# Performance work log

Hardware: AMD Instinct MI355X
Metric: run time of the kernel (lower is better)

## Reference

```python
import jax, jax.numpy as jnp
import numpy as np

B, S, C = 2, 4096, 512
H = 8            # num heads
D = C // H       # head dim = 64


def setup_inputs() -> dict:
    key = jax.random.key(0)
    ks = jax.random.split(key, 5)
    s = 0.02
    return {
        "hidden_states": jax.random.normal(ks[0], (B, S, C), dtype=jnp.float32),
        "Wq": jax.random.normal(ks[1], (C, C), dtype=jnp.float32) * s,
        "Wk": jax.random.normal(ks[2], (C, C), dtype=jnp.float32) * s,
        "Wv": jax.random.normal(ks[3], (C, C), dtype=jnp.float32) * s,
        "Wo": jax.random.normal(ks[4], (C, C), dtype=jnp.float32) * s,
        "bo": jnp.zeros((C,), dtype=jnp.float32),
    }


def reference(hidden_states, Wq, Wk, Wv, Wo, bo):
    # Self-attention path of AttnProcessor (encoder_hidden_states=None,
    # no norms, no mask, residual_connection=False, rescale=1.0).
    b, s, c = hidden_states.shape
    scale = jnp.float32(D) ** -0.5
    # QKV projections (Linear, no bias as in diffusers defaults)
    q = hidden_states @ Wq.T   # [b,s,c]
    k = hidden_states @ Wk.T
    v = hidden_states @ Wv.T
    # head_to_batch_dim: [b,s,c] -> [b,s,h,d]
    q = q.reshape(b, s, H, D)
    k = k.reshape(b, s, H, D)
    v = v.reshape(b, s, H, D)
    # get_attention_scores: scaled QK^T + softmax (full O(S^2) matrix, as in source)
    scores = jnp.einsum("bqhd,bkhd->bhqk", q, k) * scale   # [b,h,s,s]
    probs = jax.nn.softmax(scores, axis=-1)
    # bmm with V, batch_to_head_dim
    out = jnp.einsum("bhqk,bkhd->bqhd", probs, v).reshape(b, s, c)
    # to_out[0] (Linear with bias); to_out[1] is Dropout (identity at eval)
    out = out @ Wo.T + bo
    return out
```

## Files before the change

### kernel.cpp

```cpp
#include <hip/hip_runtime.h>
#include <hip/hip_bf16.h>

#define BB 2
#define SS 4096
#define CC 512
#define HH 8
#define DD 64
#define MM (BB*SS)

typedef __bf16 bf16;
typedef __attribute__((ext_vector_type(8))) __bf16 bf16x8;
typedef __attribute__((ext_vector_type(4))) __bf16 bf16x4;
typedef __attribute__((ext_vector_type(4))) float f32x4;

#define LP 72
#define QSCALE 0.18033688f

__device__ __forceinline__ bf16x8 cvt8(const float4 a, const float4 b) {
  bf16x8 r;
  r[0]=(bf16)a.x; r[1]=(bf16)a.y; r[2]=(bf16)a.z; r[3]=(bf16)a.w;
  r[4]=(bf16)b.x; r[5]=(bf16)b.y; r[6]=(bf16)b.z; r[7]=(bf16)b.w;
  return r;
}

__device__ __forceinline__ void gl16(const bf16* g, bf16* l) {
  __builtin_amdgcn_global_load_lds(
      (const __attribute__((address_space(1))) void*)g,
      (__attribute__((address_space(3))) void*)l, 16, 0, 0);
}

__global__ __launch_bounds__(256) void cvt_all(
    const float* __restrict__ hs, const float* __restrict__ Wq,
    const float* __restrict__ Wk, const float* __restrict__ Wv,
    const float* __restrict__ Wo,
    bf16* __restrict__ Xb, bf16* __restrict__ Wb, bf16* __restrict__ Wob)
{
  const size_t tid = (size_t)blockIdx.x * 256 + threadIdx.x;
  if (tid < 524288) {
    const size_t e = tid * 8;
    float4 a = ((const float4*)(hs + e))[0];
    float4 b = ((const float4*)(hs + e))[1];
    *(bf16x8*)(Xb + e) = cvt8(a, b);
  } else {
    const size_t e = (tid - 524288) * 8;
    if (e < 786432) {
      const int tens = (int)(e >> 18);
      const float* src = ((tens == 0) ? Wq : (tens == 1) ? Wk : Wv) + (e & 262143);
      const float sc = (tens == 0) ? QSCALE : 1.f;
      float4 a = ((const float4*)src)[0];
      float4 b = ((const float4*)src)[1];
      bf16x8 r;
      r[0]=(bf16)(a.x*sc); r[1]=(bf16)(a.y*sc); r[2]=(bf16)(a.z*sc); r[3]=(bf16)(a.w*sc);
      r[4]=(bf16)(b.x*sc); r[5]=(bf16)(b.y*sc); r[6]=(bf16)(b.z*sc); r[7]=(bf16)(b.w*sc);
      *(bf16x8*)(Wb + e) = r;
    } else {
      const size_t eo = e - 786432;
      float4 a = ((const float4*)(Wo + eo))[0];
      float4 b = ((const float4*)(Wo + eo))[1];
      *(bf16x8*)(Wob + eo) = cvt8(a, b);
    }
  }
}

__global__ __launch_bounds__(256) void qkv_gemm(
    const bf16* __restrict__ Xb, const bf16* __restrict__ Wb,
    bf16* __restrict__ qp, bf16* __restrict__ kp, bf16* __restrict__ vtp)
{
  __shared__ bf16 Aa[64*64];
  __shared__ bf16 Ab[64*64];
  __shared__ bf16 Ba[64*64];
  __shared__ bf16 Bb[64*64];
  const int bid = blockIdx.x;
  const int swz = (bid & 7) * 96 + (bid >> 3);
  const int m0  = (swz / 12) * 128;
  const int nf0 = (swz % 12) * 128;
  const int tens = nf0 >> 9;
  const int n0 = nf0 & 511;

  const int t = threadIdx.x;
  const int w = t >> 6;
  const int lane = t & 63;
  const int l15 = lane & 15;
  const int quad = lane >> 4;
  const int sr = lane >> 3;
  const int sc = (lane & 7) * 8;

  f32x4 acc[2][2][4];
  #pragma unroll
  for (int mi = 0; mi < 2; ++mi)
    #pragma unroll
    for (int ni = 0; ni < 2; ++ni)
      #pragma unroll
      for (int nt = 0; nt < 4; ++nt)
        #pragma unroll
        for (int r = 0; r < 4; ++r) acc[mi][ni][nt][r] = 0.f;

  for (int k0 = 0; k0 < CC; k0 += 64) {
    __syncthreads();
    {
      const bf16* pa = Xb + (size_t)(m0 + w*16 + sr) * CC + k0 + sc;
      gl16(pa,             &Aa[w*1024]);
      gl16(pa + 8*CC,      &Aa[w*1024 + 512]);
      const bf16* pb = Xb + (size_t)(m0 + 64 + w*16 + sr) * CC + k0 + sc;
      gl16(pb,             &Ab[w*1024]);
      gl16(pb + 8*CC,      &Ab[w*1024 + 512]);
      const bf16* p1 = Wb + (size_t)(nf0 + w*16 + sr) * CC + k0 + sc;
      gl16(p1,             &Ba[w*1024]);
      gl16(p1 + 8*CC,      &Ba[w*1024 + 512]);
      const bf16* p2 = Wb + (size_t)(nf0 + 64 + w*16 + sr) * CC + k0 + sc;
      gl16(p2,             &Bb[w*1024]);
      gl16(p2 + 8*CC,      &Bb[w*1024 + 512]);
    }
    __syncthreads();
    #pragma unroll
    for (int c = 0; c < 2; ++c) {
      bf16x8 afa = *(const bf16x8*)&Aa[(w*16 + l15)*64 + c*32 + quad*8];
      bf16x8 afb = *(const bf16x8*)&Ab[(w*16 + l15)*64 + c*32 + quad*8];
      #pragma unroll
      for (int nt = 0; nt < 4; ++nt) {
        bf16x8 ba = *(const bf16x8*)&Ba[(nt*16 + l15)*64 + c*32 + quad*8];
        bf16x8 bb = *(const bf16x8*)&Bb[(nt*16 + l15)*64 + c*32 + quad*8];
        acc[0][0][nt] = __builtin_amdgcn_mfma_f32_16x16x32_bf16(afa, ba, acc[0][0][nt], 0, 0, 0);
        acc[1][0][nt] = __builtin_amdgcn_mfma_f32_16x16x32_bf16(afb, ba, acc[1][0][nt], 0, 0, 0);
        acc[0][1][nt] = __builtin_amdgcn_mfma_f32_16x16x32_bf16(afa, bb, acc[0][1][nt], 0, 0, 0);
        acc[1][1][nt] = __builtin_amdgcn_mfma_f32_16x16x32_bf16(afb, bb, acc[1][1][nt], 0, 0, 0);
      }
    }
  }

  bf16* plane = (tens == 0) ? qp : ((tens == 1) ? kp : vtp);
  const int c8 = (t & 7) * 8;

  auto epi = [&](const f32x4* as, int mt0, int nb) {
    const int b = mt0 >> 12, s0g = mt0 & 4095;
    const int h = nb >> 6;
    __syncthreads();
    if (tens < 2) {
      #pragma unroll
      for (int nt = 0; nt < 4; ++nt)
        #pragma unroll
        for (int r = 0; r < 4; ++r)
          Aa[(w*16 + quad*4 + r)*64 + nt*16 + l15] = (bf16)as[nt][r];
    } else {
      #pragma unroll
      for (int nt = 0; nt < 4; ++nt)
        #pragma unroll
        for (int r = 0; r < 4; ++r)
          Aa[(nt*16 + l15)*64 + w*16 + quad*4 + r] = (bf16)as[nt][r];
    }
    __syncthreads();
    #pragma unroll
    for (int i = 0; i < 2; ++i) {
      const int row = (t >> 3) + 32*i;
      bf16x8 v = *(const bf16x8*)&Aa[row*64 + c8];
      if (tens < 2) {
        *(bf16x8*)&plane[((size_t)((b*HH + h)*SS) + s0g + row)*DD + c8] = v;
      } else {
        *(bf16x8*)&plane[((size_t)((b*HH + h)*DD) + row)*SS + s0g + c8] = v;
      }
    }
  };

  epi(acc[0][0], m0,      n0);
  epi(acc[1][0], m0 + 64, n0);
  epi(acc[0][1], m0,      n0 + 64);
  epi(acc[1][1], m0 + 64, n0 + 64);
}

__global__ __launch_bounds__(512, 4) void attn_fa(
    const bf16* __restrict__ qpl, const bf16* __restrict__ kpl,
    const bf16* __restrict__ vtpl, bf16* __restrict__ aout)
{
  __shared__ __align__(16) bf16 smem[2 * 4 * 64 * LP];

  const int t = threadIdx.x;
  const int w = t >> 6;
  const int g = w >> 2;
  const int wl = w & 3;
  const int lane = t & 63;
  const int l15 = lane & 15;
  const int quad = lane >> 4;

  const int lin = blockIdx.x;
  const int bh = lin & 15;
  const int q0 = (lin >> 4) * 128;
  const size_t plane = (size_t)SS * DD;
  const bf16* Qp = qpl + (size_t)bh * plane;
  const bf16* Kp = kpl + (size_t)bh * plane;
  const bf16* Vg = vtpl + (size_t)bh * plane;

  bf16* Ktg = smem + g * (4*64*LP);
  bf16* Vtg = Ktg + 2*64*LP;

  bf16x8 qf[2][2];
  #pragma unroll
  for (int wq = 0; wq < 2; ++wq) {
    const bf16* qr = Qp + (size_t)(q0 + wl*32 + wq*16 + l15) * DD + quad*8;
    qf[wq][0] = *(const bf16x8*)qr;
    qf[wq][1] = *(const bf16x8*)(qr + 32);
  }

  f32x4 o[2][4];
  f32x4 osum[2];
  #pragma unroll
  for (int wq = 0; wq < 2; ++wq) {
    #pragma unroll
    for (int nt = 0; nt < 4; ++nt)
      #pragma unroll
      for (int r = 0; r < 4; ++r) o[wq][nt][r] = 0.f;
    #pragma unroll
    for (int r = 0; r < 4; ++r) osum[wq][r] = 0.f;
  }

  bf16x8 ones;
  #pragma unroll
  for (int i = 0; i < 8; ++i) ones[i] = (bf16)1.0f;

  const int t8  = t & 255;
  const int r0s = t8 >> 2;
  const int cs  = (t8 & 3) << 4;
  const int K0  = ((t8 & 1) << 3) + (((t8 >> 1) & 1) << 5);
  const int kbase = g << 11;

  bf16x8 ka0, ka1, va, vb;
  {
    ka0 = *(const bf16x8*)&Kp[(size_t)(kbase + r0s)*DD + cs];
    ka1 = *(const bf16x8*)&Kp[(size_t)(kbase + r0s)*DD + cs + 8];
    va  = *(const bf16x8*)&Vg[(size_t)r0s*SS + kbase + K0];
    vb  = *(const bf16x8*)&Vg[(size_t)r0s*SS + kbase + K0 + 16];
    *(bf16x8*)&Ktg[r0s*LP + cs]     = ka0;
    *(bf16x8*)&Ktg[r0s*LP + cs + 8] = ka1;
    bf16x8 vv;
    vv[0]=va[0]; vv[1]=va[1]; vv[2]=va[2]; vv[3]=va[3];
    vv[4]=vb[0]; vv[5]=vb[1]; vv[6]=vb[2]; vv[7]=vb[3];
    *(bf16x8*)&Vtg[r0s*LP + cs] = vv;
    vv[0]=va[4]; vv[1]=va[5]; vv[2]=va[6]; vv[3]=va[7];
    vv[4]=vb[4]; vv[5]=vb[5]; vv[6]=vb[6]; vv[7]=vb[7];
    *(bf16x8*)&Vtg[r0s*LP + cs + 8] = vv;
  }
  __syncthreads();

  for (int it = 0; it < 32; ++it) {
    const int cur = it & 1;
    if (it < 31) {
      const int kn = kbase + (it + 1) * 64;
      ka0 = *(const bf16x8*)&Kp[(size_t)(kn + r0s)*DD + cs];
      ka1 = *(const bf16x8*)&Kp[(size_t)(kn + r0s)*DD + cs + 8];
      va  = *(const bf16x8*)&Vg[(size_t)r0s*SS + kn + K0];
      vb  = *(const bf16x8*)&Vg[(size_t)r0s*SS + kn + K0 + 16];
    }

    const bf16* Ktc = Ktg + cur*(64*LP);
    const bf16* Vtc = Vtg + cur*(64*LP);

    f32x4 st[2][4];
    __builtin_amdgcn_s_setprio(1);
    #pragma unroll
    for (int nt = 0; nt < 4; ++nt) {
      bf16x8 kf0 = *(const bf16x8*)&Ktc[(nt*16 + l15)*LP + quad*8];
      bf16x8 kf1 = *(const bf16x8*)&Ktc[(nt*16 + l15)*LP + 32 + quad*8];
      #pragma unroll
      for (int wq = 0; wq < 2; ++wq) {
        f32x4 z; z[0]=z[1]=z[2]=z[3]=0.f;
        z = __builtin_amdgcn_mfma_f32_16x16x32_bf16(kf0, qf[wq][0], z, 0, 0, 0);
        z = __builtin_amdgcn_mfma_f32_16x16x32_bf16(kf1, qf[wq][1], z, 0, 0, 0);
        st[wq][nt] = z;
      }
    }
    __builtin_amdgcn_s_setprio(0);

    bf16x8 pb0[2];
    #pragma unroll
    for (int wq = 0; wq < 2; ++wq)
      #pragma unroll
      for (int nt = 0; nt < 2; ++nt)
        #pragma unroll
        for (int r = 0; r < 4; ++r)
          pb0[wq][(nt & 1)*4 + r] = (bf16)__builtin_amdgcn_exp2f(st[wq][nt][r]);

    __builtin_amdgcn_s_setprio(1);
    #pragma unroll
    for (int nt = 0; nt < 4; ++nt) {
      bf16x8 vf = *(const bf16x8*)&Vtc[(nt*16 + l15)*LP + quad*8];
      #pragma unroll
      for (int wq = 0; wq < 2; ++wq)
        o[wq][nt] = __builtin_amdgcn_mfma_f32_16x16x32_bf16(vf, pb0[wq], o[wq][nt], 0, 0, 0);
    }
    #pragma unroll
    for (int wq = 0; wq < 2; ++wq)
      osum[wq] = __builtin_amdgcn_mfma_f32_16x16x32_bf16(ones, pb0[wq], osum[wq], 0, 0, 0);
    __builtin_amdgcn_s_setprio(0);

    bf16x8 pb1[2];
    #pragma unroll
    for (int wq = 0; wq < 2; ++wq)
      #pragma unroll
      for (int nt = 2; nt < 4; ++nt)
        #pragma unroll
        for (int r = 0; r < 4; ++r)
          pb1[wq][(nt & 1)*4 + r] = (bf16)__builtin_amdgcn_exp2f(st[wq][nt][r]);

    __builtin_amdgcn_s_setprio(1);
    #pragma unroll
    for (int nt = 0; nt < 4; ++nt) {
      bf16x8 vf = *(const bf16x8*)&Vtc[(nt*16 + l15)*LP + 32 + quad*8];
      #pragma unroll
      for (int wq = 0; wq < 2; ++wq)
        o[wq][nt] = __builtin_amdgcn_mfma_f32_16x16x32_bf16(vf, pb1[wq], o[wq][nt], 0, 0, 0);
    }
    #pragma unroll
    for (int wq = 0; wq < 2; ++wq)
      osum[wq] = __builtin_amdgcn_mfma_f32_16x16x32_bf16(ones, pb1[wq], osum[wq], 0, 0, 0);
    __builtin_amdgcn_s_setprio(0);

    if (it < 31) {
      const int nxt = cur ^ 1;
      bf16* Ktn = Ktg + nxt*(64*LP);
      bf16* Vtn = Vtg + nxt*(64*LP);
      *(bf16x8*)&Ktn[r0s*LP + cs]     = ka0;
      *(bf16x8*)&Ktn[r0s*LP + cs + 8] = ka1;
      bf16x8 vv;
      vv[0]=va[0]; vv[1]=va[1]; vv[2]=va[2]; vv[3]=va[3];
      vv[4]=vb[0]; vv[5]=vb[1]; vv[6]=vb[2]; vv[7]=vb[3];
      *(bf16x8*)&Vtn[r0s*LP + cs] = vv;
      vv[0]=va[4]; vv[1]=va[5]; vv[2]=va[6]; vv[3]=va[7];
      vv[4]=vb[4]; vv[5]=vb[5]; vv[6]=vb[6]; vv[7]=vb[7];
      *(bf16x8*)&Vtn[r0s*LP + cs + 8] = vv;
      __syncthreads();
    }
  }

  __syncthreads();
  float* stash = (float*)smem;
  const int sidx = (wl*64 + lane) * 36;
  if (g == 1) {
    #pragma unroll
    for (int wq = 0; wq < 2; ++wq)
      #pragma unroll
      for (int nt = 0; nt < 4; ++nt)
        *(f32x4*)&stash[sidx + (wq*4 + nt)*4] = o[wq][nt];
    stash[sidx + 32] = osum[0][0];
    stash[sidx + 33] = osum[1][0];
  }
  __syncthreads();
  if (g == 0) {
    #pragma unroll
    for (int wq = 0; wq < 2; ++wq)
      #pragma unroll
      for (int nt = 0; nt < 4; ++nt) {
        f32x4 p = *(const f32x4*)&stash[sidx + (wq*4 + nt)*4];
        #pragma unroll
        for (int r = 0; r < 4; ++r) o[wq][nt][r] += p[r];
      }
    const float s0 = osum[0][0] + stash[sidx + 32];
    const float s1 = osum[1][0] + stash[sidx + 33];

    const int b = bh >> 3, h = bh & 7;
    #pragma unroll
    for (int wq = 0; wq < 2; ++wq) {
      const float inv = 1.f / (wq == 0 ? s0 : s1);
      const size_t row = (size_t)(b*SS + q0 + wl*32 + wq*16 + l15) * CC + h*DD;
      #pragma unroll
      for (int nt = 0; nt < 4; ++nt) {
        bf16x4 ov;
        #pragma unroll
        for (int r = 0; r < 4; ++r) ov[r] = (bf16)(o[wq][nt][r] * inv);
        *(bf16x4*)&aout[row + nt*16 + quad*4] = ov;
      }
    }
  }
}

__global__ __launch_bounds__(256) void out_gemm(
    const bf16* __restrict__ A, const bf16* __restrict__ Wob,
    const float* __restrict__ bo, float* __restrict__ out)
{
  __shared__ bf16 Aa[64*64];
  __shared__ bf16 Ab[64*64];
  __shared__ bf16 Bt[64*64];
  const int bid = blockIdx.x;
  const int swz = (bid & 7) * 64 + (bid >> 3);
  const int m0 = (swz >> 3) * 128;
  const int n0 = (swz & 7) * 64;

  const int t = threadIdx.x;
  const int w = t >> 6;
  const int lane = t & 63;
  const int l15 = lane & 15;
  const int quad = lane >> 4;
  const int sr = lane >> 3;
  const int sc = (lane & 7) * 8;

  f32x4 aca[4], acb[4];
  #pragma unroll
  for (int i = 0; i < 4; ++i)
    #pragma unroll
    for (int j = 0; j < 4; ++j) { aca[i][j] = 0.f; acb[i][j] = 0.f; }

  for (int k0 = 0; k0 < CC; k0 += 64) {
    __syncthreads();
    {
      const bf16* pa = A + (size_t)(m0 + w*16 + sr) * CC + k0 + sc;
      gl16(pa,        &Aa[w*1024]);
      gl16(pa + 8*CC, &Aa[w*1024 + 512]);
      const bf16* pb = A + (size_t)(m0 + 64 + w*16 + sr) * CC + k0 + sc;
      gl16(pb,        &Ab[w*1024]);
      gl16(pb + 8*CC, &Ab[w*1024 + 512]);
      const bf16* p1 = Wob + (size_t)(n0 + w*16 + sr) * CC + k0 + sc;
      gl16(p1,        &Bt[w*1024]);
      gl16(p1 + 8*CC, &Bt[w*1024 + 512]);
    }
    __syncthreads();
    #pragma unroll
    for (int c = 0; c < 2; ++c) {
      bf16x8 afa = *(const bf16x8*)&Aa[(w*16 + l15)*64 + c*32 + quad*8];
      bf16x8 afb = *(const bf16x8*)&Ab[(w*16 + l15)*64 + c*32 + quad*8];
      #pragma unroll
      for (int nt = 0; nt < 4; ++nt) {
        bf16x8 bfr = *(const bf16x8*)&Bt[(nt*16 + l15)*64 + c*32 + quad*8];
        aca[nt] = __builtin_amdgcn_mfma_f32_16x16x32_bf16(afa, bfr, aca[nt], 0, 0, 0);
        acb[nt] = __builtin_amdgcn_mfma_f32_16x16x32_bf16(afb, bfr, acb[nt], 0, 0, 0);
      }
    }
  }

  #pragma unroll
  for (int nt = 0; nt < 4; ++nt) {
    const int ng = n0 + nt*16 + l15;
    const float bias = bo[ng];
    #pragma unroll
    for (int r = 0; r < 4; ++r) {
      const int mga = m0 + w*16 + quad*4 + r;
      out[(size_t)mga*CC + ng] = aca[nt][r] + bias;
      const int mgb = m0 + 64 + w*16 + quad*4 + r;
      out[(size_t)mgb*CC + ng] = acb[nt][r] + bias;
    }
  }
}

extern "C" void kernel_launch(void* const* d_in, const int* in_sizes, int n_in,
                              void* d_out, int out_size, void* d_ws, size_t ws_size,
                              hipStream_t stream) {
  const float* hs = (const float*)d_in[0];
  const float* Wq = (const float*)d_in[1];
  const float* Wk = (const float*)d_in[2];
  const float* Wv = (const float*)d_in[3];
  const float* Wo = (const float*)d_in[4];
  const float* bo = (const float*)d_in[5];
  float* out = (float*)d_out;

  const size_t PE = (size_t)BB*HH*SS*DD;
  bf16* ws   = (bf16*)d_ws;
  bf16* qp   = ws;
  bf16* kp   = ws + PE;
  bf16* vtp  = ws + 2*PE;
  bf16* Xb   = ws + 3*PE;
  bf16* aout = ws + 3*PE;
  bf16* Wb   = ws + 4*PE;
  bf16* Wob  = Wb + 786432;

  cvt_all <<<dim3(2560), 256, 0, stream>>>(hs, Wq, Wk, Wv, Wo, Xb, Wb, Wob);
  qkv_gemm<<<dim3(768),  256, 0, stream>>>(Xb, Wb, qp, kp, vtp);
  attn_fa <<<dim3(512),  512, 0, stream>>>(qp, kp, vtp, aout);
  out_gemm<<<dim3(512),  256, 0, stream>>>(aout, Wob, bo, out);
}
```

Measured before the change: 191.0 us.

## Fuse activation fp32-to-bf16 conversion into QKV GEMM and coalesce output stores

After: 192.9 us. Within noise of the previous version (+1.0%).

```diff
diff --git a/kernel.cpp b/kernel.cpp
--- a/kernel.cpp
+++ b/kernel.cpp
@@ -29,45 +29,36 @@
       (__attribute__((address_space(3))) void*)l, 16, 0, 0);
 }
 
-__global__ __launch_bounds__(256) void cvt_all(
-    const float* __restrict__ hs, const float* __restrict__ Wq,
-    const float* __restrict__ Wk, const float* __restrict__ Wv,
-    const float* __restrict__ Wo,
-    bf16* __restrict__ Xb, bf16* __restrict__ Wb, bf16* __restrict__ Wob)
+__global__ __launch_bounds__(256) void cvt_w(
+    const float* __restrict__ Wq, const float* __restrict__ Wk,
+    const float* __restrict__ Wv, const float* __restrict__ Wo,
+    bf16* __restrict__ Wb, bf16* __restrict__ Wob)
 {
-  const size_t tid = (size_t)blockIdx.x * 256 + threadIdx.x;
-  if (tid < 524288) {
-    const size_t e = tid * 8;
-    float4 a = ((const float4*)(hs + e))[0];
-    float4 b = ((const float4*)(hs + e))[1];
-    *(bf16x8*)(Xb + e) = cvt8(a, b);
+  size_t e = ((size_t)blockIdx.x * 256 + threadIdx.x) * 8;
+  if (e < 786432) {
+    const int tens = (int)(e >> 18);
+    const float* src = ((tens == 0) ? Wq : (tens == 1) ? Wk : Wv) + (e & 262143);
+    const float sc = (tens == 0) ? QSCALE : 1.f;
+    float4 a = ((const float4*)src)[0];
+    float4 b = ((const float4*)src)[1];
+    bf16x8 r;
+    r[0]=(bf16)(a.x*sc); r[1]=(bf16)(a.y*sc); r[2]=(bf16)(a.z*sc); r[3]=(bf16)(a.w*sc);
+    r[4]=(bf16)(b.x*sc); r[5]=(bf16)(b.y*sc); r[6]=(bf16)(b.z*sc); r[7]=(bf16)(b.w*sc);
+    *(bf16x8*)(Wb + e) = r;
   } else {
-    const size_t e = (tid - 524288) * 8;
-    if (e < 786432) {
-      const int tens = (int)(e >> 18);
-      const float* src = ((tens == 0) ? Wq : (tens == 1) ? Wk : Wv) + (e & 262143);
-      const float sc = (tens == 0) ? QSCALE : 1.f;
-      float4 a = ((const float4*)src)[0];
-      float4 b = ((const float4*)src)[1];
-      bf16x8 r;
-      r[0]=(bf16)(a.x*sc); r[1]=(bf16)(a.y*sc); r[2]=(bf16)(a.z*sc); r[3]=(bf16)(a.w*sc);
-      r[4]=(bf16)(b.x*sc); r[5]=(bf16)(b.y*sc); r[6]=(bf16)(b.z*sc); r[7]=(bf16)(b.w*sc);
-      *(bf16x8*)(Wb + e) = r;
-    } else {
-      const size_t eo = e - 786432;
-      float4 a = ((const float4*)(Wo + eo))[0];
-      float4 b = ((const float4*)(Wo + eo))[1];
-      *(bf16x8*)(Wob + eo) = cvt8(a, b);
-    }
+    const size_t eo = e - 786432;
+    float4 a = ((const float4*)(Wo + eo))[0];
+    float4 b = ((const float4*)(Wo + eo))[1];
+    *(bf16x8*)(Wob + eo) = cvt8(a, b);
   }
 }
 
 __global__ __launch_bounds__(256) void qkv_gemm(
-    const bf16* __restrict__ Xb, const bf16* __restrict__ Wb,
+    const float* __restrict__ hs, const bf16* __restrict__ Wb,
     bf16* __restrict__ qp, bf16* __restrict__ kp, bf16* __restrict__ vtp)
 {
-  __shared__ bf16 Aa[64*64];
-  __shared__ bf16 Ab[64*64];
+  __shared__ bf16 Aa[64*LP];
+  __shared__ bf16 Ab[64*LP];
   __shared__ bf16 Ba[64*64];
   __shared__ bf16 Bb[64*64];
   const int bid = blockIdx.x;
@@ -82,6 +73,8 @@
   const int lane = t & 63;
   const int l15 = lane & 15;
   const int quad = lane >> 4;
+  const int srow = t >> 2;
+  const int scol = (t & 3) << 4;
   const int sr = lane >> 3;
   const int sc = (lane & 7) * 8;
 
@@ -98,24 +91,32 @@
   for (int k0 = 0; k0 < CC; k0 += 64) {
     __syncthreads();
     {
-      const bf16* pa = Xb + (size_t)(m0 + w*16 + sr) * CC + k0 + sc;
-      gl16(pa,             &Aa[w*1024]);
-      gl16(pa + 8*CC,      &Aa[w*1024 + 512]);
-      const bf16* pb = Xb + (size_t)(m0 + 64 + w*16 + sr) * CC + k0 + sc;
-      gl16(pb,             &Ab[w*1024]);
-      gl16(pb + 8*CC,      &Ab[w*1024 + 512]);
+      const float* pa = hs + (size_t)(m0 + srow) * CC + k0 + scol;
+      float4 a0 = ((const float4*)pa)[0];
+      float4 a1 = ((const float4*)pa)[1];
+      float4 a2 = ((const float4*)pa)[2];
+      float4 a3 = ((const float4*)pa)[3];
+      *(bf16x8*)&Aa[srow*LP + scol]     = cvt8(a0, a1);
+      *(bf16x8*)&Aa[srow*LP + scol + 8] = cvt8(a2, a3);
+      const float* pb = hs + (size_t)(m0 + 64 + srow) * CC + k0 + scol;
+      float4 b0 = ((const float4*)pb)[0];
+      float4 b1 = ((const float4*)pb)[1];
+      float4 b2 = ((const float4*)pb)[2];
+      float4 b3 = ((const float4*)pb)[3];
+      *(bf16x8*)&Ab[srow*LP + scol]     = cvt8(b0, b1);
+      *(bf16x8*)&Ab[srow*LP + scol + 8] = cvt8(b2, b3);
       const bf16* p1 = Wb + (size_t)(nf0 + w*16 + sr) * CC + k0 + sc;
-      gl16(p1,             &Ba[w*1024]);
-      gl16(p1 + 8*CC,      &Ba[w*1024 + 512]);
+      gl16(p1,        &Ba[w*1024]);
+      gl16(p1 + 8*CC, &Ba[w*1024 + 512]);
       const bf16* p2 = Wb + (size_t)(nf0 + 64 + w*16 + sr) * CC + k0 + sc;
-      gl16(p2,             &Bb[w*1024]);
-      gl16(p2 + 8*CC,      &Bb[w*1024 + 512]);
+      gl16(p2,        &Bb[w*1024]);
+      gl16(p2 + 8*CC, &Bb[w*1024 + 512]);
     }
     __syncthreads();
     #pragma unroll
     for (int c = 0; c < 2; ++c) {
-      bf16x8 afa = *(const bf16x8*)&Aa[(w*16 + l15)*64 + c*32 + quad*8];
-      bf16x8 afb = *(const bf16x8*)&Ab[(w*16 + l15)*64 + c*32 + quad*8];
+      bf16x8 afa = *(const bf16x8*)&Aa[(w*16 + l15)*LP + c*32 + quad*8];
+      bf16x8 afb = *(const bf16x8*)&Ab[(w*16 + l15)*LP + c*32 + quad*8];
       #pragma unroll
       for (int nt = 0; nt < 4; ++nt) {
         bf16x8 ba = *(const bf16x8*)&Ba[(nt*16 + l15)*64 + c*32 + quad*8];
@@ -140,19 +141,19 @@
       for (int nt = 0; nt < 4; ++nt)
         #pragma unroll
         for (int r = 0; r < 4; ++r)
-          Aa[(w*16 + quad*4 + r)*64 + nt*16 + l15] = (bf16)as[nt][r];
+          Aa[(w*16 + quad*4 + r)*LP + nt*16 + l15] = (bf16)as[nt][r];
     } else {
       #pragma unroll
       for (int nt = 0; nt < 4; ++nt)
         #pragma unroll
         for (int r = 0; r < 4; ++r)
-          Aa[(nt*16 + l15)*64 + w*16 + quad*4 + r] = (bf16)as[nt][r];
+          Aa[(nt*16 + l15)*LP + w*16 + quad*4 + r] = (bf16)as[nt][r];
     }
     __syncthreads();
     #pragma unroll
     for (int i = 0; i < 2; ++i) {
       const int row = (t >> 3) + 32*i;
-      bf16x8 v = *(const bf16x8*)&Aa[row*64 + c8];
+      bf16x8 v = *(const bf16x8*)&Aa[row*LP + c8];
       if (tens < 2) {
         *(bf16x8*)&plane[((size_t)((b*HH + h)*SS) + s0g + row)*DD + c8] = v;
       } else {
@@ -375,9 +376,12 @@
     const bf16* __restrict__ A, const bf16* __restrict__ Wob,
     const float* __restrict__ bo, float* __restrict__ out)
 {
-  __shared__ bf16 Aa[64*64];
-  __shared__ bf16 Ab[64*64];
-  __shared__ bf16 Bt[64*64];
+  __shared__ __align__(16) bf16 smem[3 * 64 * 64];
+  bf16* Aa = smem;
+  bf16* Ab = smem + 4096;
+  bf16* Bt = smem + 8192;
+  float* stash = (float*)smem;
+
   const int bid = blockIdx.x;
   const int swz = (bid & 7) * 64 + (bid >> 3);
   const int m0 = (swz >> 3) * 128;
@@ -424,16 +428,27 @@
     }
   }
 
-  #pragma unroll
-  for (int nt = 0; nt < 4; ++nt) {
-    const int ng = n0 + nt*16 + l15;
-    const float bias = bo[ng];
-    #pragma unroll
-    for (int r = 0; r < 4; ++r) {
-      const int mga = m0 + w*16 + quad*4 + r;
-      out[(size_t)mga*CC + ng] = aca[nt][r] + bias;
-      const int mgb = m0 + 64 + w*16 + quad*4 + r;
-      out[(size_t)mgb*CC + ng] = acb[nt][r] + bias;
+  const int erow = t >> 2;
+  const int ecol = (t & 3) * 16;
+  float bias[4];
+  #pragma unroll
+  for (int nt = 0; nt < 4; ++nt) bias[nt] = bo[n0 + nt*16 + l15];
+
+  #pragma unroll
+  for (int half = 0; half < 2; ++half) {
+    const f32x4* as = half ? acb : aca;
+    __syncthreads();
+    #pragma unroll
+    for (int nt = 0; nt < 4; ++nt)
+      #pragma unroll
+      for (int r = 0; r < 4; ++r)
+        stash[(w*16 + quad*4 + r)*68 + nt*16 + l15] = as[nt][r] + bias[nt];
+    __syncthreads();
+    float* orow = out + (size_t)(m0 + half*64 + erow) * CC + n0 + ecol;
+    #pragma unroll
+    for (int j = 0; j < 4; ++j) {
+      float4 v = *(const float4*)&stash[erow*68 + ecol + 4*j];
+      ((float4*)orow)[j] = v;
     }
   }
 }
@@ -454,13 +469,12 @@
   bf16* qp   = ws;
   bf16* kp   = ws + PE;
   bf16* vtp  = ws + 2*PE;
-  bf16* Xb   = ws + 3*PE;
   bf16* aout = ws + 3*PE;
   bf16* Wb   = ws + 4*PE;
   bf16* Wob  = Wb + 786432;
 
-  cvt_all <<<dim3(2560), 256, 0, stream>>>(hs, Wq, Wk, Wv, Wo, Xb, Wb, Wob);
-  qkv_gemm<<<dim3(768),  256, 0, stream>>>(Xb, Wb, qp, kp, vtp);
-  attn_fa <<<dim3(512),  512, 0, stream>>>(qp, kp, vtp, aout);
-  out_gemm<<<dim3(512),  256, 0, stream>>>(aout, Wob, bo, out);
-}
+  cvt_w   <<<dim3(512), 256, 0, stream>>>(Wq, Wk, Wv, Wo, Wb, Wob);
+  qkv_gemm<<<dim3(768), 256, 0, stream>>>(hs, Wb, qp, kp, vtp);
+  attn_fa <<<dim3(512), 512, 0, stream>>>(qp, kp, vtp, aout);
+  out_gemm<<<dim3(512), 256, 0, stream>>>(aout, Wob, bo, out);
+}
```
